# Optimization experiments

Measured on AMD Instinct MI355X. Metric: run time of the kernel, lower is better.

The kernel has to match this reference:

```python
import jax, jax.numpy as jnp
import numpy as np
import math

CS = 8       # cell_size
NBINS = 8
SIGMA = 1.0
IMG = 224
BATCH = 256
TWO_PI = 2.0 * math.pi


def setup_inputs() -> dict:
    key = jax.random.key(0)
    x = jax.random.normal(key, (BATCH, 3, IMG, IMG), dtype=jnp.float32)
    coords = jnp.arange(CS, dtype=jnp.float32) - (CS - 1) / 2.0
    xx, yy = jnp.meshgrid(coords, coords, indexing='ij')
    gauss = jnp.exp(-(xx ** 2 + yy ** 2) / (2.0 * SIGMA ** 2)).reshape(1, CS * CS)
    kx = jnp.array([[-1., 0., 1.], [-2., 0., 2.], [-1., 0., 1.]], dtype=jnp.float32).reshape(1, 1, 3, 3)
    ky = jnp.array([[-1., -2., -1.], [0., 0., 0.], [1., 2., 1.]], dtype=jnp.float32).reshape(1, 1, 3, 3)
    return {"x": x, "gauss": gauss, "kx": kx, "ky": ky}


def _conv(im, k):
    # NCHW conv, padding=1, stride=1 (matches F.conv2d(..., padding=1))
    return jax.lax.conv_general_dilated(
        im, k, window_strides=(1, 1), padding=[(1, 1), (1, 1)],
        dimension_numbers=('NCHW', 'OIHW', 'NCHW'))


def reference(x, gauss, kx, ky):
    bs, _, H, W = x.shape
    gray = 0.2989 * x[:, 0:1] + 0.587 * x[:, 1:2] + 0.114 * x[:, 2:3]  # [bs,1,H,W]
    gx = _conv(gray, kx)
    gy = _conv(gray, ky)
    mag = jnp.sqrt(gx ** 2 + gy ** 2 + 1e-6)
    ang = jnp.mod(jnp.arctan2(gy, gx), TWO_PI)
    Hc, Wc = H // CS, W // CS
    n_cells = Hc * Wc

    def to_cells(a):
        # [bs,1,H,W] -> [bs*n_cells, CS*CS], within-cell order (kh,kw) row-major
        # matching F.unfold's kernel-position ordering.
        return a.reshape(bs, Hc, CS, Wc, CS).transpose(0, 1, 3, 2, 4).reshape(bs * n_cells, CS * CS)

    mags = to_cells(mag) * gauss  # gauss broadcasts over kernel positions
    angs = to_cells(ang)

    bin_w = TWO_PI / NBINS
    idx = (angs / bin_w).astype(jnp.int32) % NBINS  # [bs*n_cells, CS*CS]

    N = bs * n_cells
    hist = jnp.zeros((N, NBINS), dtype=mags.dtype)
    hist = hist.at[jnp.arange(N)[:, None], idx].add(mags)  # scatter_add per cell
    hist = hist.reshape(bs, n_cells * NBINS)
    hist = hist / (jnp.linalg.norm(hist, axis=1, keepdims=True) + 1e-6)
    return hist
```

## Files before the change

### kernel.cpp

```cpp
#include <hip/hip_runtime.h>
#include <math.h>

#define NBINS 8
#define IMG 224
#define HC 28
#define OUTPER (HC*HC*NBINS)
#define BATCH 256
#define PL (IMG*IMG)

template<bool EDGE>
__device__ __forceinline__ void load_gray(const float* __restrict__ xb,
    int r0, int c0, int cl, int lane, float v[10], float& hl, float& hr)
{
    #pragma unroll
    for (int j = 0; j < 10; ++j) {
        int gr  = r0 - 1 + j;
        int grc = EDGE ? (gr < 0 ? 0 : (gr > IMG - 1 ? IMG - 1 : gr)) : gr;
        const float* p = xb + grc * IMG + cl;
        float gv = 0.2989f * p[0] + 0.587f * p[PL] + 0.114f * p[2 * PL];
        v[j] = (EDGE && (gr < 0 || gr > IMG - 1)) ? 0.f : gv;
    }
    {
        int jl = lane - 54; jl = jl < 0 ? 0 : (jl > 9 ? 9 : jl);
        int gr = r0 - 1 + jl;
        int grc = EDGE ? (gr < 0 ? 0 : (gr > IMG - 1 ? IMG - 1 : gr)) : gr;
        int colL = c0 - 1; bool zc = colL < 0; int colc = zc ? 0 : colL;
        const float* p = xb + grc * IMG + colc;
        float gv = 0.2989f * p[0] + 0.587f * p[PL] + 0.114f * p[2 * PL];
        hl = (zc || (EDGE && (gr < 0 || gr > IMG - 1))) ? 0.f : gv;
    }
    {
        int jr = lane - 44; jr = jr < 0 ? 0 : (jr > 9 ? 9 : jr);
        int gr = r0 - 1 + jr;
        int grc = EDGE ? (gr < 0 ? 0 : (gr > IMG - 1 ? IMG - 1 : gr)) : gr;
        int colR = c0 + 64; bool zc = colR > IMG - 1; int colc = zc ? IMG - 1 : colR;
        const float* p = xb + grc * IMG + colc;
        float gv = 0.2989f * p[0] + 0.587f * p[PL] + 0.114f * p[2 * PL];
        hr = (zc || (EDGE && (gr < 0 || gr > IMG - 1))) ? 0.f : gv;
    }
}

__global__ __launch_bounds__(256) void hog_main_kernel(
    const float* __restrict__ x, const float* __restrict__ gauss,
    float* __restrict__ out, float* __restrict__ partial)
{
    __shared__ float hist[4][64];

    const int tid  = threadIdx.x;
    const int wv   = tid >> 6;
    const int lane = tid & 63;
    const int bc   = blockIdx.x;
    const int b    = bc / HC;
    const int cr   = bc - b * HC;
    const int r0   = cr * 8;
    const int c0   = wv * 64;
    const int c    = c0 + lane;
    const int cl   = c > IMG - 1 ? IMG - 1 : c;

    const float* xb = x + (size_t)b * 3 * PL;

    hist[wv][lane] = 0.f;

    float v[10], hl, hr;
    if (cr == 0 || cr == HC - 1) load_gray<true >(xb, r0, c0, cl, lane, v, hl, hr);
    else                         load_gray<false>(xb, r0, c0, cl, lane, v, hl, hr);

    const int wc = lane & 7;
    float tt = (float)wc - 3.5f;
    float gw = __builtin_amdgcn_exp2f(-(tt * tt) * 0.72134752f);
    const float EROW[8] = { 0.0021874911f, 0.043936934f, 0.32465247f, 0.88249690f,
                            0.88249690f, 0.32465247f, 0.043936934f, 0.0021874911f };

    float* cellp = &hist[wv][(lane >> 3) << 3];

    auto mklr = [&](int j, float& lf, float& rt) {
        float a = __shfl_up(v[j], 1, 64);
        float hLj = __shfl(hl, 54 + j, 64);
        lf = (lane == 0) ? hLj : a;
        float d = __shfl_down(v[j], 1, 64);
        float hRj = __shfl(hr, 44 + j, 64);
        d = (lane == 63) ? hRj : d;
        rt = (c >= IMG - 1) ? 0.f : d;
    };

    float tL, tC, tR, mL, mC, mR;
    mklr(0, tL, tR); tC = v[0];
    mklr(1, mL, mR); mC = v[1];

    #pragma unroll
    for (int sr = 0; sr < 8; ++sr) {
        float bL, bR, bC = v[sr + 2];
        mklr(sr + 2, bL, bR);

        float gx = (tR - tL) + 2.f * (mR - mL) + (bR - bL);
        float gy = (bL - tL) + 2.f * (bC - tC) + (bR - tR);
        float mag = __builtin_amdgcn_sqrtf(gx * gx + gy * gy + 1e-6f);
        float ax = fabsf(gx), ay = fabsf(gy);

        int bin;
        if (gy > 0.f)       bin = (gx > 0.f)  ? ((gy < gx) ? 0 : 1)
                                : (gx == 0.f) ? 2 : ((ay > ax) ? 2 : 3);
        else if (gy == 0.f) bin = (gx < 0.f) ? 4 : 0;
        else                bin = (gx < 0.f)  ? ((ay < ax) ? 4 : 5)
                                : (gx == 0.f) ? 6 : ((ay > ax) ? 6 : 7);

        float wm = EROW[sr] * (gw * mag);
        atomicAdd(cellp + bin, wm);

        tL = mL; tC = mC; tR = mR;
        mL = bL; mC = bC; mR = bR;
    }

    asm volatile("s_waitcnt lgkmcnt(0)" ::: "memory");
    float val = hist[wv][lane];

    float ssq = 0.f;
    if (c < IMG) {
        out[(size_t)b * OUTPER + (size_t)cr * IMG + c] = val;
        ssq = val * val;
    }

    #pragma unroll
    for (int o = 32; o > 0; o >>= 1) ssq += __shfl_down(ssq, o, 64);
    if (lane == 0) partial[bc * 4 + wv] = ssq;
}

__global__ __launch_bounds__(256) void hog_norm_kernel(
    float* __restrict__ out, const float* __restrict__ partial)
{
    const int bq = blockIdx.x, tid = threadIdx.x;
    const int b = bq >> 2, q = bq & 3;
    __shared__ float wsum[4];
    __shared__ float s_inv;
    float s = (tid < HC * 4) ? partial[b * HC * 4 + tid] : 0.f;
    #pragma unroll
    for (int o = 32; o > 0; o >>= 1) s += __shfl_down(s, o, 64);
    if ((tid & 63) == 0) wsum[tid >> 6] = s;
    __syncthreads();
    if (tid == 0) {
        float t = wsum[0] + wsum[1] + wsum[2] + wsum[3];
        s_inv = 1.0f / (sqrtf(t) + 1e-6f);
    }
    __syncthreads();
    float inv = s_inv;
    float4* o4 = (float4*)(out + (size_t)b * OUTPER + (size_t)q * (OUTPER / 4));
    for (int i = tid; i < OUTPER / 16; i += 256) {
        float4 w = o4[i];
        w.x *= inv; w.y *= inv; w.z *= inv; w.w *= inv;
        o4[i] = w;
    }
}

extern "C" void kernel_launch(void* const* d_in, const int* in_sizes, int n_in,
                              void* d_out, int out_size, void* d_ws, size_t ws_size,
                              hipStream_t stream) {
    const float* x     = (const float*)d_in[0];
    const float* gauss = (const float*)d_in[1];
    float* out     = (float*)d_out;
    float* partial = (float*)d_ws;

    hog_main_kernel<<<BATCH * HC, 256, 0, stream>>>(x, gauss, out, partial);
    hog_norm_kernel<<<BATCH * 4, 256, 0, stream>>>(out, partial);
}
```

Before: 264.6 us.

## Give each lane four pixels via float4 loads and keep histograms in registers

Each wave now handles one full cell row, and each lane loads four adjacent columns with float4 loads. This replaces the per-column scalar loads and the separate halo loads. The separable Sobel sums are shared across the four pixels, so only two shuffles per row are needed. Histograms are built in eight private registers per lane and merged between lane pairs with a DPP swap, which removes the LDS atomics. The cost is more register pressure from the float4 rows and the unrolled per-bin select-adds, plus a launch reshaped to 7 blocks per image.

```diff
diff --git a/kernel.cpp b/kernel.cpp
--- a/kernel.cpp
+++ b/kernel.cpp
@@ -8,35 +8,32 @@
 #define BATCH 256
 #define PL (IMG*IMG)
 
+__device__ __forceinline__ float dpp_swap1(float x) {
+    return __int_as_float(__builtin_amdgcn_update_dpp(
+        0, __float_as_int(x), 0xB1, 0xF, 0xF, false));
+}
+
 template<bool EDGE>
 __device__ __forceinline__ void load_gray(const float* __restrict__ xb,
-    int r0, int c0, int cl, int lane, float v[10], float& hl, float& hr)
+                                          int r0, int col4, int lane,
+                                          float4 v[10])
 {
     #pragma unroll
     for (int j = 0; j < 10; ++j) {
         int gr  = r0 - 1 + j;
         int grc = EDGE ? (gr < 0 ? 0 : (gr > IMG - 1 ? IMG - 1 : gr)) : gr;
-        const float* p = xb + grc * IMG + cl;
-        float gv = 0.2989f * p[0] + 0.587f * p[PL] + 0.114f * p[2 * PL];
-        v[j] = (EDGE && (gr < 0 || gr > IMG - 1)) ? 0.f : gv;
-    }
-    {
-        int jl = lane - 54; jl = jl < 0 ? 0 : (jl > 9 ? 9 : jl);
-        int gr = r0 - 1 + jl;
-        int grc = EDGE ? (gr < 0 ? 0 : (gr > IMG - 1 ? IMG - 1 : gr)) : gr;
-        int colL = c0 - 1; bool zc = colL < 0; int colc = zc ? 0 : colL;
-        const float* p = xb + grc * IMG + colc;
-        float gv = 0.2989f * p[0] + 0.587f * p[PL] + 0.114f * p[2 * PL];
-        hl = (zc || (EDGE && (gr < 0 || gr > IMG - 1))) ? 0.f : gv;
-    }
-    {
-        int jr = lane - 44; jr = jr < 0 ? 0 : (jr > 9 ? 9 : jr);
-        int gr = r0 - 1 + jr;
-        int grc = EDGE ? (gr < 0 ? 0 : (gr > IMG - 1 ? IMG - 1 : gr)) : gr;
-        int colR = c0 + 64; bool zc = colR > IMG - 1; int colc = zc ? IMG - 1 : colR;
-        const float* p = xb + grc * IMG + colc;
-        float gv = 0.2989f * p[0] + 0.587f * p[PL] + 0.114f * p[2 * PL];
-        hr = (zc || (EDGE && (gr < 0 || gr > IMG - 1))) ? 0.f : gv;
+        const float* p = xb + grc * IMG + col4;
+        float4 R = *(const float4*)(p);
+        float4 G = *(const float4*)(p + PL);
+        float4 B = *(const float4*)(p + 2 * PL);
+        float4 g;
+        g.x = 0.2989f * R.x + 0.587f * G.x + 0.114f * B.x;
+        g.y = 0.2989f * R.y + 0.587f * G.y + 0.114f * B.y;
+        g.z = 0.2989f * R.z + 0.587f * G.z + 0.114f * B.z;
+        g.w = 0.2989f * R.w + 0.587f * G.w + 0.114f * B.w;
+        bool z = (lane >= 56) || (EDGE && (gr < 0 || gr > IMG - 1));
+        if (z) { g.x = 0.f; g.y = 0.f; g.z = 0.f; g.w = 0.f; }
+        v[j] = g;
     }
 }
 
@@ -44,85 +41,87 @@
     const float* __restrict__ x, const float* __restrict__ gauss,
     float* __restrict__ out, float* __restrict__ partial)
 {
-    __shared__ float hist[4][64];
-
     const int tid  = threadIdx.x;
     const int wv   = tid >> 6;
     const int lane = tid & 63;
     const int bc   = blockIdx.x;
-    const int b    = bc / HC;
-    const int cr   = bc - b * HC;
+    const int b    = bc / 7;
+    const int cr   = (bc - b * 7) * 4 + wv;
     const int r0   = cr * 8;
-    const int c0   = wv * 64;
-    const int c    = c0 + lane;
-    const int cl   = c > IMG - 1 ? IMG - 1 : c;
+    const int li   = lane < 55 ? lane : 55;
+    const int col4 = li * 4;
 
     const float* xb = x + (size_t)b * 3 * PL;
 
-    hist[wv][lane] = 0.f;
+    float4 v[10];
+    if (cr == 0 || cr == HC - 1) load_gray<true >(xb, r0, col4, lane, v);
+    else                         load_gray<false>(xb, r0, col4, lane, v);
 
-    float v[10], hl, hr;
-    if (cr == 0 || cr == HC - 1) load_gray<true >(xb, r0, c0, cl, lane, v, hl, hr);
-    else                         load_gray<false>(xb, r0, c0, cl, lane, v, hl, hr);
+    const float E0 = 0.0021874911f, E1 = 0.043936934f,
+                E2 = 0.32465247f,   E3 = 0.88249690f;
+    const bool odd = (lane & 1);
+    const float ew0 = odd ? E3 : E0, ew1 = odd ? E2 : E1,
+                ew2 = odd ? E1 : E2, ew3 = odd ? E0 : E3;
+    const float EROW[8] = { E0, E1, E2, E3, E3, E2, E1, E0 };
 
-    const int wc = lane & 7;
-    float tt = (float)wc - 3.5f;
-    float gw = __builtin_amdgcn_exp2f(-(tt * tt) * 0.72134752f);
-    const float EROW[8] = { 0.0021874911f, 0.043936934f, 0.32465247f, 0.88249690f,
-                            0.88249690f, 0.32465247f, 0.043936934f, 0.0021874911f };
+    float h[8];
+    #pragma unroll
+    for (int k = 0; k < 8; ++k) h[k] = 0.f;
 
-    float* cellp = &hist[wv][(lane >> 3) << 3];
-
-    auto mklr = [&](int j, float& lf, float& rt) {
-        float a = __shfl_up(v[j], 1, 64);
-        float hLj = __shfl(hl, 54 + j, 64);
-        lf = (lane == 0) ? hLj : a;
-        float d = __shfl_down(v[j], 1, 64);
-        float hRj = __shfl(hr, 44 + j, 64);
-        d = (lane == 63) ? hRj : d;
-        rt = (c >= IMG - 1) ? 0.f : d;
-    };
-
-    float tL, tC, tR, mL, mC, mR;
-    mklr(0, tL, tR); tC = v[0];
-    mklr(1, mL, mR); mC = v[1];
-
-    #pragma unroll
-    for (int sr = 0; sr < 8; ++sr) {
-        float bL, bR, bC = v[sr + 2];
-        mklr(sr + 2, bL, bR);
-
-        float gx = (tR - tL) + 2.f * (mR - mL) + (bR - bL);
-        float gy = (bL - tL) + 2.f * (bC - tC) + (bR - tR);
+    auto pix = [&](float gx, float gy, float w) {
         float mag = __builtin_amdgcn_sqrtf(gx * gx + gy * gy + 1e-6f);
         float ax = fabsf(gx), ay = fabsf(gy);
-
         int bin;
         if (gy > 0.f)       bin = (gx > 0.f)  ? ((gy < gx) ? 0 : 1)
                                 : (gx == 0.f) ? 2 : ((ay > ax) ? 2 : 3);
         else if (gy == 0.f) bin = (gx < 0.f) ? 4 : 0;
         else                bin = (gx < 0.f)  ? ((ay < ax) ? 4 : 5)
                                 : (gx == 0.f) ? 6 : ((ay > ax) ? 6 : 7);
+        float wm = w * mag;
+        #pragma unroll
+        for (int k = 0; k < 8; ++k) h[k] += (bin == k) ? wm : 0.f;
+    };
 
-        float wm = EROW[sr] * (gw * mag);
-        atomicAdd(cellp + bin, wm);
+    #pragma unroll
+    for (int sr = 0; sr < 8; ++sr) {
+        float4 t = v[sr], m = v[sr + 1], bt = v[sr + 2];
+        float4 s, d;
+        s.x = t.x + 2.f * m.x + bt.x;  s.y = t.y + 2.f * m.y + bt.y;
+        s.z = t.z + 2.f * m.z + bt.z;  s.w = t.w + 2.f * m.w + bt.w;
+        d.x = bt.x - t.x;  d.y = bt.y - t.y;
+        d.z = bt.z - t.z;  d.w = bt.w - t.w;
 
-        tL = mL; tC = mC; tR = mR;
-        mL = bL; mC = bC; mR = bR;
+        float sL = __shfl_up(s.w, 1, 64);   sL = (lane == 0) ? 0.f : sL;
+        float dL = __shfl_up(d.w, 1, 64);   dL = (lane == 0) ? 0.f : dL;
+        float sR = __shfl_down(s.x, 1, 64);
+        float dR = __shfl_down(d.x, 1, 64);
+
+        float gx0 = s.y - sL,  gx1 = s.z - s.x,
+              gx2 = s.w - s.y, gx3 = sR  - s.z;
+        float gy0 = dL  + 2.f * d.x + d.y, gy1 = d.x + 2.f * d.y + d.z,
+              gy2 = d.y + 2.f * d.z + d.w, gy3 = d.z + 2.f * d.w + dR;
+
+        float er = EROW[sr];
+        pix(gx0, gy0, er * ew0);
+        pix(gx1, gy1, er * ew1);
+        pix(gx2, gy2, er * ew2);
+        pix(gx3, gy3, er * ew3);
     }
 
-    asm volatile("s_waitcnt lgkmcnt(0)" ::: "memory");
-    float val = hist[wv][lane];
+    #pragma unroll
+    for (int k = 0; k < 8; ++k) h[k] += dpp_swap1(h[k]);
 
     float ssq = 0.f;
-    if (c < IMG) {
-        out[(size_t)b * OUTPER + (size_t)cr * IMG + c] = val;
-        ssq = val * val;
+    if (lane < 56) {
+        float4 st = odd ? make_float4(h[4], h[5], h[6], h[7])
+                        : make_float4(h[0], h[1], h[2], h[3]);
+        *(float4*)(out + (size_t)b * OUTPER + (size_t)cr * IMG + 4 * lane) = st;
+        ssq = st.x * st.x + st.y * st.y + st.z * st.z + st.w * st.w;
     }
 
     #pragma unroll
     for (int o = 32; o > 0; o >>= 1) ssq += __shfl_down(ssq, o, 64);
-    if (lane == 0) partial[bc * 4 + wv] = ssq;
+    if (lane == 0) partial[b * HC + cr] = ssq;
 }
 
 __global__ __launch_bounds__(256) void hog_norm_kernel(
@@ -132,7 +131,7 @@
     const int b = bq >> 2, q = bq & 3;
     __shared__ float wsum[4];
     __shared__ float s_inv;
-    float s = (tid < HC * 4) ? partial[b * HC * 4 + tid] : 0.f;
+    float s = (tid < HC) ? partial[b * HC + tid] : 0.f;
     #pragma unroll
     for (int o = 32; o > 0; o >>= 1) s += __shfl_down(s, o, 64);
     if ((tid & 63) == 0) wsum[tid >> 6] = s;
@@ -159,6 +158,6 @@
     float* out     = (float*)d_out;
     float* partial = (float*)d_ws;
 
-    hog_main_kernel<<<BATCH * HC, 256, 0, stream>>>(x, gauss, out, partial);
+    hog_main_kernel<<<BATCH * 7, 256, 0, stream>>>(x, gauss, out, partial);
     hog_norm_kernel<<<BATCH * 4, 256, 0, stream>>>(out, partial);
 }
```

Result: faster. 230.8 us (-12.8%).
